# Kernel optimization log

Hardware: AMD Instinct MI355X
Metric: run time of the kernel (lower is better)

Reference implementation:

```python
import jax, jax.numpy as jnp
from jax import lax
import numpy as np

B, CIN, COUT, H, W = 16, 128, 256, 64, 64
E, K, RED = 4, 3, 4

def setup_inputs() -> dict:
    key = jax.random.key(0)
    ks = jax.random.split(key, 16)
    s = 0.05
    return {
        'x': jax.random.normal(ks[0], (B, CIN, H, W), jnp.float32),
        'expert_w': jax.random.normal(ks[1], (E, COUT, CIN, K, K), jnp.float32) * s,
        'r1_w': jax.random.normal(ks[2], (E // 2, CIN), jnp.float32) * s,
        'r1_b': jnp.zeros((E // 2,), jnp.float32),
        'r2_w': jax.random.normal(ks[3], (E, E // 2), jnp.float32) * s,
        'r2_b': jnp.zeros((E,), jnp.float32),
        'r3_w': jax.random.normal(ks[4], (E, E), jnp.float32) * s,
        'r3_b': jnp.zeros((E,), jnp.float32),
        'ca1_w': jax.random.normal(ks[5], (COUT // RED, COUT), jnp.float32) * s,
        'ca1_b': jnp.zeros((COUT // RED,), jnp.float32),
        'ca2_w': jax.random.normal(ks[6], (COUT, COUT // RED), jnp.float32) * s,
        'ca2_b': jnp.zeros((COUT,), jnp.float32),
        'sa_w': jax.random.normal(ks[7], (1, COUT, 7, 7), jnp.float32) * s,
        'sa_b': jnp.zeros((1,), jnp.float32),
        'bn_gamma': jnp.ones((COUT,), jnp.float32),
        'bn_beta': jnp.zeros((COUT,), jnp.float32),
    }

def _conv(x, w, stride, pad):
    return lax.conv_general_dilated(x, w, (stride, stride), [(pad, pad), (pad, pad)],
                                     dimension_numbers=('NCHW', 'OIHW', 'NCHW'))

def reference(x, expert_w, r1_w, r1_b, r2_w, r2_b, r3_w, r3_b,
              ca1_w, ca1_b, ca2_w, ca2_b, sa_w, sa_b, bn_gamma, bn_beta):
    # --- routing: GAP -> 1x1 convs (as matmuls) -> softmax over experts ---
    g = x.mean(axis=(2, 3))                                   # [B, Cin]
    h = jax.nn.relu(g @ r1_w.T + r1_b)
    h = jax.nn.relu(h @ r2_w.T + r2_b)
    rw = jax.nn.softmax(h @ r3_w.T + r3_b, axis=1)            # [B, E]
    # --- all experts as one stacked conv, then weighted combine ---
    w = expert_w.reshape(E * COUT, CIN, K, K)
    y = _conv(x, w, 1, 1)                                     # [B, E*Cout, H, W]
    y = y.reshape(x.shape[0], E, COUT, y.shape[2], y.shape[3])
    out = jnp.einsum('be,bechw->bchw', rw, y)                 # [B, Cout, H, W]
    # --- channel attention (SE) ---
    p = out.mean(axis=(2, 3))                                  # [B, Cout]
    ca = jax.nn.sigmoid(jax.nn.relu(p @ ca1_w.T + ca1_b) @ ca2_w.T + ca2_b)
    # --- spatial attention: 7x7 conv -> sigmoid ---
    sa = jax.nn.sigmoid(_conv(out, sa_w, 1, 3) + sa_b[None, :, None, None])  # [B,1,H,W]
    out = out * ca[:, :, None, None] * sa
    # --- BatchNorm (training mode: batch statistics) + ReLU ---
    mean = out.mean(axis=(0, 2, 3))
    var = out.var(axis=(0, 2, 3))
    out = (out - mean[None, :, None, None]) * lax.rsqrt(var + 1e-5)[None, :, None, None]
    out = out * bn_gamma[None, :, None, None] + bn_beta[None, :, None, None]
    return jax.nn.relu(out)
```

## Files before the change

kernel.cpp:

```cpp
#include <hip/hip_runtime.h>
#include <math.h>

#define B_    16
#define CIN_  128
#define COUT_ 256
#define H_    64
#define W_    64
#define HW_   4096

typedef __attribute__((ext_vector_type(8))) short short8v;
typedef __attribute__((ext_vector_type(4))) float f32x4;

#define WS_GPX     0
#define WS_RW      131072
#define WS_CP      131136
#define WS_CA      196672
#define WS_BNSCALE 208960
#define WS_BNSHIFT 209216
#define WS_SA      209472
#define WS_WSA     275008
#define WS_WCB_F   283200
#define WS_XT_F    2642496
#define WS_U_F     WS_XT_F
#define WS_MIX_F   7103040

static __device__ __forceinline__ unsigned short f2bf(float f) {
    union { float f; unsigned int u; } v; v.f = f;
    unsigned int u = v.u;
    return (unsigned short)((u + 0x7FFFu + ((u >> 16) & 1u)) >> 16);
}
static __device__ __forceinline__ float bf2f(unsigned short h) {
    union { unsigned int u; float f; } v; v.u = ((unsigned int)h) << 16;
    return v.f;
}

__device__ __forceinline__ void gl16(const void* g, const void* l) {
    __builtin_amdgcn_global_load_lds(
        (const __attribute__((address_space(1))) unsigned int*)g,
        (__attribute__((address_space(3))) unsigned int*)l, 16, 0, 0);
}

__global__ __launch_bounds__(256) void k_xt(const float* __restrict__ x,
                                            unsigned short* __restrict__ xt,
                                            float* __restrict__ gpart) {
    int wg = blockIdx.x + (blockIdx.y << 6);
    int nw = ((wg & 7) << 7) + (wg >> 3);
    int h = nw & 63, b = nw >> 6;
    int t = threadIdx.x;
    int w = t & 63, c8 = t >> 6;
    unsigned short* xtb = xt + (size_t)b * 66*66*128;
    unsigned short* orow = xtb + (((size_t)(h+1))*66 + (w+1))*128;
    float* gp = gpart + ((size_t)b*64 + h)*128;
    #pragma unroll
    for (int i = 0; i < 4; ++i) {
        int ci0 = i*32 + c8*8;
        float f[8];
        short8v vv;
        #pragma unroll
        for (int j = 0; j < 8; ++j) {
            f[j] = x[(((size_t)b*CIN_ + ci0 + j)*H_ + h)*W_ + w];
            vv[j] = (short)f2bf(f[j]);
        }
        *(short8v*)(orow + ci0) = vv;
        #pragma unroll
        for (int j = 0; j < 8; ++j) {
            float s = f[j];
            s += __shfl_down(s, 32, 64);
            s += __shfl_down(s, 16, 64);
            s += __shfl_down(s, 8, 64);
            s += __shfl_down(s, 4, 64);
            s += __shfl_down(s, 2, 64);
            s += __shfl_down(s, 1, 64);
            f[j] = s;
        }
        if (w == 0) {
            #pragma unroll
            for (int j = 0; j < 8; ++j) gp[ci0 + j] = f[j];
        }
    }
    xtb[(((size_t)(h+1))*66 + (t >> 7)*65)*128 + (t & 127)] = 0;
    if (h == 0 || h == 63) {
        int r = (h == 0) ? 0 : 65;
        unsigned short* rowp = xtb + ((size_t)r*66)*128;
        for (int i = t; i < 1056; i += 256)
            *(short8v*)(rowp + (size_t)i*8) = (short8v){0,0,0,0,0,0,0,0};
    }
}

__global__ void k_route(const float* __restrict__ gpart,
                        const float* r1w, const float* r1b,
                        const float* r2w, const float* r2b,
                        const float* r3w, const float* r3b,
                        float* __restrict__ rw) {
    int b = blockIdx.x;
    int t = threadIdx.x;
    __shared__ float gl_[128];
    float s = 0.f;
    for (int h = 0; h < 64; ++h) s += gpart[((size_t)b*64 + h)*128 + t];
    gl_[t] = s * (1.f/4096.f);
    __syncthreads();
    if (t == 0) {
        float h1[2];
        for (int j = 0; j < 2; ++j) {
            float acc = r1b[j];
            for (int c = 0; c < CIN_; ++c) acc += gl_[c]*r1w[j*CIN_+c];
            h1[j] = fmaxf(acc, 0.f);
        }
        float h2[4];
        for (int e = 0; e < 4; ++e)
            h2[e] = fmaxf(r2b[e] + h1[0]*r2w[e*2] + h1[1]*r2w[e*2+1], 0.f);
        float lg[4], m = -1e30f;
        for (int e = 0; e < 4; ++e) {
            float acc = r3b[e];
            for (int j = 0; j < 4; ++j) acc += h2[j]*r3w[e*4+j];
            lg[e] = acc; m = fmaxf(m, acc);
        }
        float den = 0.f;
        for (int e = 0; e < 4; ++e) { lg[e] = expf(lg[e]-m); den += lg[e]; }
        float inv = 1.f/den;
        for (int e = 0; e < 4; ++e) rw[b*4+e] = lg[e]*inv;
    }
}

__global__ __launch_bounds__(256) void k_wcomb(const float* __restrict__ ew,
                                               const float* __restrict__ rw,
                                               unsigned short* __restrict__ wc,
                                               const float* __restrict__ saw,
                                               unsigned short* __restrict__ wsa) {
    int t = threadIdx.x;
    if (blockIdx.x >= COUT_) {
        int i = (blockIdx.x - COUT_)*256 + t;
        int tap = i >> 8, c = i & 255;
        float v = (tap < 49) ? saw[c*49 + tap] : 0.f;
        wsa[tap*256 + c] = f2bf(v);
        return;
    }
    int co = blockIdx.x;
    __shared__ float ewl[4*1152];
    __shared__ float rwl[64];
    #pragma unroll
    for (int e = 0; e < 4; ++e) {
        const float* src = ew + ((size_t)(e*COUT_ + co))*1152;
        for (int i = t; i < 1152; i += 256) ewl[e*1152 + i] = src[i];
    }
    if (t < 64) rwl[t] = rw[t];
    __syncthreads();
    for (int i = 0; i < 72; ++i) {
        int f = i*256 + t;
        int b = f / 1152;
        int rem = f - b*1152;
        int tap = rem >> 7, ci = rem & 127;
        int lidx = ci*9 + tap;
        float v = rwl[b*4+0]*ewl[0*1152+lidx] + rwl[b*4+1]*ewl[1*1152+lidx]
                + rwl[b*4+2]*ewl[2*1152+lidx] + rwl[b*4+3]*ewl[3*1152+lidx];
        wc[((size_t)(b*9 + tap)*COUT_ + co)*128 + ci] = f2bf(v);
    }
}

__global__ __launch_bounds__(256) void k_conv(const unsigned short* __restrict__ xt,
                                              const unsigned short* __restrict__ wc,
                                              unsigned short* __restrict__ mixb,
                                              float* __restrict__ cpart) {
    __shared__ unsigned short xs[1600*8];
    __shared__ unsigned short wl[2304*8];
    __shared__ float gsl[4][64];
    int wg = blockIdx.x + (blockIdx.y << 4) + (blockIdx.z << 6);
    int nw = ((wg & 7) << 7) + (wg >> 3);
    int ht = nw & 15;
    int cb = (nw >> 4) & 3;
    int b  = nw >> 6;
    int t  = threadIdx.x;
    int wv = t >> 6, lane = t & 63;
    int lr = lane & 15, kq = lane >> 4;
    int h0 = ht * 4;

    const unsigned short* xtb = xt + (size_t)b * 66*66*128;
    const unsigned short* wcb = wc + (size_t)b * 9*256*128;

    f32x4 acc[4][4];
    #pragma unroll
    for (int m = 0; m < 4; ++m)
        #pragma unroll
        for (int n = 0; n < 4; ++n) acc[m][n] = (f32x4){0.f,0.f,0.f,0.f};

    for (int ci0 = 0; ci0 < CIN_; ci0 += 32) {
        __syncthreads();
        for (int j = wv; j < 25; j += 4) {
            int s = j*64 + lane;
            if (s > 1583) s = 1583;
            int pos = s >> 2, q = s & 3;
            int rp = pos / 66, cp = pos - rp*66;
            const unsigned short* g = xtb + (((size_t)(h0 + rp)*66 + cp)*128 + ci0 + q*8);
            gl16(g, (const char*)xs + (size_t)j*1024);
        }
        for (int j = wv; j < 36; j += 4) {
            int s = j*64 + lane;
            int tap = s >> 8, col = (s >> 2) & 63, q = s & 3;
            const unsigned short* g = wcb + (((size_t)tap*COUT_ + cb*64 + col)*128 + ci0 + q*8);
            gl16(g, (const char*)wl + (size_t)j*1024);
        }
        asm volatile("s_waitcnt vmcnt(0)" ::: "memory");
        __syncthreads();

        #pragma unroll
        for (int dh = 0; dh < 3; ++dh) {
            #pragma unroll
            for (int dw = 0; dw < 3; ++dw) {
                int tap = dh*3 + dw;
                short8v af[4], bfv[4];
                #pragma unroll
                for (int m = 0; m < 4; ++m)
                    af[m] = *(const short8v*)(wl + ((size_t)tap*2048 + (m*16 + lr)*32 + kq*8));
                #pragma unroll
                for (int n = 0; n < 4; ++n)
                    bfv[n] = *(const short8v*)(xs + ((size_t)(wv+dh)*2112 + (n*16 + lr + dw)*32 + kq*8));
                #pragma unroll
                for (int m = 0; m < 4; ++m)
                    #pragma unroll
                    for (int n = 0; n < 4; ++n)
                        acc[m][n] = __builtin_amdgcn_mfma_f32_16x16x32_bf16(
                            af[m], bfv[n], acc[m][n], 0, 0, 0);
            }
        }
    }

    unsigned short* ob = mixb + ((size_t)b*COUT_ + cb*64)*HW_ + (h0 + wv)*W_;
    #pragma unroll
    for (int m = 0; m < 4; ++m)
        #pragma unroll
        for (int n = 0; n < 4; ++n) {
            f32x4 v = acc[m][n];
            #pragma unroll
            for (int r = 0; r < 4; ++r)
                ob[(size_t)(m*16 + kq*4 + r)*HW_ + n*16 + lr] = f2bf(v[r]);
        }

    float gp[4][4];
    #pragma unroll
    for (int m = 0; m < 4; ++m)
        #pragma unroll
        for (int r = 0; r < 4; ++r)
            gp[m][r] = acc[m][0][r] + acc[m][1][r] + acc[m][2][r] + acc[m][3][r];
    #pragma unroll
    for (int o = 8; o > 0; o >>= 1)
        #pragma unroll
        for (int m = 0; m < 4; ++m)
            #pragma unroll
            for (int r = 0; r < 4; ++r)
                gp[m][r] += __shfl_down(gp[m][r], o, 64);
    if ((lane & 15) == 0) {
        #pragma unroll
        for (int m = 0; m < 4; ++m)
            #pragma unroll
            for (int r = 0; r < 4; ++r)
                gsl[wv][m*16 + kq*4 + r] = gp[m][r];
    }
    __syncthreads();
    if (t < 64) {
        float s = gsl[0][t] + gsl[1][t] + gsl[2][t] + gsl[3][t];
        cpart[((size_t)b*16 + ht)*COUT_ + cb*64 + t] = s;
    }
}

__global__ __launch_bounds__(256) void k_sa_gemm(const unsigned short* __restrict__ mixb,
                                                 const unsigned short* __restrict__ wsa,
                                                 float* __restrict__ u) {
    __shared__ unsigned short wl[16384];
    __shared__ unsigned short bt[16384];
    int wg = blockIdx.x + (blockIdx.y << 6);
    int nw = ((wg & 7) << 7) + (wg >> 3);
    int pxt = nw & 63;
    int b   = nw >> 6;
    int t = threadIdx.x, wv = t >> 6, lane = t & 63;
    int lr = lane & 15, kq = lane >> 4;
    int px0 = pxt * 64;

    #pragma unroll
    for (int k = 0; k < 8; ++k) {
        int s = t + k*256;
        int row = s >> 5, cs = s & 31;
        short8v v = *(const short8v*)(wsa + row*256 + cs*8);
        int off = row*512 + ((cs*16) ^ ((row & 7) << 4));
        *(short8v*)((char*)wl + off) = v;
    }
    {
        int px = lane;
        const unsigned short* mb = mixb + (size_t)b*COUT_*HW_ + px0 + px;
        #pragma unroll
        for (int c8 = 0; c8 < 8; ++c8) {
            int cb = wv*64 + c8*8;
            short8v v;
            #pragma unroll
            for (int j = 0; j < 8; ++j)
                v[j] = (short)mb[(size_t)(cb + j)*HW_];
            int off = px*512 + ((cb*2) ^ ((px & 7) << 4));
            *(short8v*)((char*)bt + off) = v;
        }
    }
    __syncthreads();

    f32x4 acc[4];
    #pragma unroll
    for (int n = 0; n < 4; ++n) acc[n] = (f32x4){0.f,0.f,0.f,0.f};

    #pragma unroll
    for (int ks = 0; ks < 8; ++ks) {
        int ci0 = ks*32;
        int arow = wv*16 + lr;
        short8v a = *(const short8v*)((const char*)wl +
                        arow*512 + (((ci0 + kq*8)*2) ^ ((arow & 7) << 4)));
        #pragma unroll
        for (int n = 0; n < 4; ++n) {
            int prow = n*16 + lr;
            short8v bv = *(const short8v*)((const char*)bt +
                            prow*512 + (((ci0 + kq*8)*2) ^ ((prow & 7) << 4)));
            acc[n] = __builtin_amdgcn_mfma_f32_16x16x32_bf16(a, bv, acc[n], 0, 0, 0);
        }
    }

    float* ub = u + (size_t)b*64*HW_;
    #pragma unroll
    for (int n = 0; n < 4; ++n)
        #pragma unroll
        for (int r = 0; r < 4; ++r)
            ub[(size_t)(wv*16 + kq*4 + r)*HW_ + px0 + n*16 + lr] = acc[n][r];
}

__global__ void k_sared_ca(const float* __restrict__ u, const float* __restrict__ sab,
                           float* __restrict__ sa,
                           const float* __restrict__ cpart,
                           const float* __restrict__ ca1w, const float* __restrict__ ca1b,
                           const float* __restrict__ ca2w, const float* __restrict__ ca2b,
                           float* __restrict__ ca) {
    int wg = blockIdx.x + (blockIdx.y << 4);
    int nw = ((wg & 7) << 5) + (wg >> 3);
    int hg = nw & 15;
    int b  = nw >> 4;
    int t = threadIdx.x;
    {
        int h = hg * 4 + (t >> 6);
        int w = t & 63;
        float s = sab[0];
        const float* ub = u + (size_t)b*64*HW_;
        #pragma unroll
        for (int dh = 0; dh < 7; ++dh) {
            int hh = h + dh - 3;
            if (hh < 0 || hh >= H_) continue;
            #pragma unroll
            for (int dw = 0; dw < 7; ++dw) {
                int ww = w + dw - 3;
                if (ww < 0 || ww >= W_) continue;
                s += ub[(size_t)(dh*7 + dw)*HW_ + hh*W_ + ww];
            }
        }
        sa[(size_t)b*HW_ + h*W_ + w] = 1.f/(1.f + expf(-s));
    }
    if (hg == 0) {
        __shared__ float pfull[256];
        __shared__ float h1[64];
        float s0 = 0.f;
        for (int h = 0; h < 16; ++h) s0 += cpart[((size_t)b*16 + h)*COUT_ + t];
        pfull[t] = s0 * (1.f/(float)HW_);
        __syncthreads();
        if (t < 64) {
            float s = ca1b[t];
            for (int c = 0; c < COUT_; ++c) s += pfull[c] * ca1w[t*COUT_ + c];
            h1[t] = fmaxf(s, 0.f);
        }
        __syncthreads();
        float s2 = ca2b[t];
        for (int j = 0; j < 64; ++j) s2 += h1[j] * ca2w[t*64 + j];
        ca[b*COUT_ + t] = 1.f/(1.f + expf(-s2));
    }
}

__global__ void k_statsfin(const unsigned short* __restrict__ mixb,
                           const float* __restrict__ ca, const float* __restrict__ sa,
                           const float* __restrict__ gamma, const float* __restrict__ beta,
                           float* __restrict__ scale, float* __restrict__ shift) {
    int c = blockIdx.x;
    int t = threadIdx.x;
    float s = 0.f, sq = 0.f;
    for (int b = 0; b < B_; ++b) {
        float cav = ca[b*COUT_ + c];
        const unsigned short* pl = mixb + ((size_t)b*COUT_ + c) * HW_;
        const float* sab = sa + (size_t)b * HW_;
        for (int i = t; i < HW_/8; i += 256) {
            short8v v = ((const short8v*)pl)[i];
            float4 w0 = ((const float4*)sab)[2*i];
            float4 w1 = ((const float4*)sab)[2*i+1];
            float f0 = bf2f((unsigned short)v[0])*cav*w0.x;
            float f1 = bf2f((unsigned short)v[1])*cav*w0.y;
            float f2 = bf2f((unsigned short)v[2])*cav*w0.z;
            float f3 = bf2f((unsigned short)v[3])*cav*w0.w;
            float f4 = bf2f((unsigned short)v[4])*cav*w1.x;
            float f5 = bf2f((unsigned short)v[5])*cav*w1.y;
            float f6 = bf2f((unsigned short)v[6])*cav*w1.z;
            float f7 = bf2f((unsigned short)v[7])*cav*w1.w;
            s  += f0+f1+f2+f3+f4+f5+f6+f7;
            sq += f0*f0+f1*f1+f2*f2+f3*f3+f4*f4+f5*f5+f6*f6+f7*f7;
        }
    }
    for (int o = 32; o > 0; o >>= 1) { s += __shfl_down(s,o,64); sq += __shfl_down(sq,o,64); }
    __shared__ float ls[8];
    int wid = t >> 6, lane = t & 63;
    if (lane == 0) { ls[wid] = s; ls[4+wid] = sq; }
    __syncthreads();
    if (t == 0) {
        float ts = ls[0]+ls[1]+ls[2]+ls[3];
        float tq = ls[4]+ls[5]+ls[6]+ls[7];
        float n = (float)(B_*HW_);
        float mean = ts/n;
        float var = tq/n - mean*mean;
        float sc = gamma[c] * rsqrtf(var + 1e-5f);
        scale[c] = sc;
        shift[c] = beta[c] - mean*sc;
    }
}

__global__ void k_bnapply(const unsigned short* __restrict__ mixb, float* __restrict__ out,
                          const float* __restrict__ ca, const float* __restrict__ sa,
                          const float* __restrict__ scale, const float* __restrict__ shift) {
    int wg = blockIdx.x;
    int nw = ((wg & 7) << 10) + (wg >> 3);
    size_t i = (size_t)nw * 256 + threadIdx.x;
    int c = (int)((i >> 9) & 255);
    int b = (int)(i >> 17);
    int px8 = (int)(i & 511);
    float cav = ca[b*COUT_ + c];
    float sc = scale[c], sh = shift[c];
    short8v v = ((const short8v*)mixb)[i];
    const float4* sp = (const float4*)(sa + (size_t)b*HW_) + (size_t)px8*2;
    float4 w0 = sp[0], w1 = sp[1];
    float4 o0, o1;
    o0.x = fmaxf(fmaf(bf2f((unsigned short)v[0])*cav*w0.x, sc, sh), 0.f);
    o0.y = fmaxf(fmaf(bf2f((unsigned short)v[1])*cav*w0.y, sc, sh), 0.f);
    o0.z = fmaxf(fmaf(bf2f((unsigned short)v[2])*cav*w0.z, sc, sh), 0.f);
    o0.w = fmaxf(fmaf(bf2f((unsigned short)v[3])*cav*w0.w, sc, sh), 0.f);
    o1.x = fmaxf(fmaf(bf2f((unsigned short)v[4])*cav*w1.x, sc, sh), 0.f);
    o1.y = fmaxf(fmaf(bf2f((unsigned short)v[5])*cav*w1.y, sc, sh), 0.f);
    o1.z = fmaxf(fmaf(bf2f((unsigned short)v[6])*cav*w1.z, sc, sh), 0.f);
    o1.w = fmaxf(fmaf(bf2f((unsigned short)v[7])*cav*w1.w, sc, sh), 0.f);
    ((float4*)out)[i*2]   = o0;
    ((float4*)out)[i*2+1] = o1;
}

extern "C" void kernel_launch(void* const* d_in, const int* in_sizes, int n_in,
                              void* d_out, int out_size, void* d_ws, size_t ws_size,
                              hipStream_t stream) {
    const float* x    = (const float*)d_in[0];
    const float* ew   = (const float*)d_in[1];
    const float* r1w  = (const float*)d_in[2];
    const float* r1b  = (const float*)d_in[3];
    const float* r2w  = (const float*)d_in[4];
    const float* r2b  = (const float*)d_in[5];
    const float* r3w  = (const float*)d_in[6];
    const float* r3b  = (const float*)d_in[7];
    const float* ca1w = (const float*)d_in[8];
    const float* ca1b = (const float*)d_in[9];
    const float* ca2w = (const float*)d_in[10];
    const float* ca2b = (const float*)d_in[11];
    const float* saw  = (const float*)d_in[12];
    const float* sab  = (const float*)d_in[13];
    const float* gm   = (const float*)d_in[14];
    const float* bt   = (const float*)d_in[15];
    float* out = (float*)d_out;
    float* ws  = (float*)d_ws;
    unsigned short* wcb  = (unsigned short*)(ws + WS_WCB_F);
    unsigned short* xt   = (unsigned short*)(ws + WS_XT_F);
    unsigned short* wsa  = (unsigned short*)(ws + WS_WSA);
    unsigned short* mixb = (unsigned short*)(ws + WS_MIX_F);
    float* u = ws + WS_U_F;

    k_xt<<<dim3(64,16), 256, 0, stream>>>(x, xt, ws+WS_GPX);
    k_route<<<16, 128, 0, stream>>>(ws+WS_GPX, r1w, r1b, r2w, r2b, r3w, r3b, ws+WS_RW);
    k_wcomb<<<320, 256, 0, stream>>>(ew, ws+WS_RW, wcb, saw, wsa);
    k_conv<<<dim3(16,4,16), 256, 0, stream>>>(xt, wcb, mixb, ws+WS_CP);
    k_sa_gemm<<<dim3(64,16), 256, 0, stream>>>(mixb, wsa, u);
    k_sared_ca<<<dim3(16,16), 256, 0, stream>>>(u, sab, ws+WS_SA, ws+WS_CP,
                                                ca1w, ca1b, ca2w, ca2b, ws+WS_CA);
    k_statsfin<<<256, 256, 0, stream>>>(mixb, ws+WS_CA, ws+WS_SA, gm, bt,
                                        ws+WS_BNSCALE, ws+WS_BNSHIFT);
    k_bnapply<<<8192, 256, 0, stream>>>(mixb, out, ws+WS_CA, ws+WS_SA,
                                        ws+WS_BNSCALE, ws+WS_BNSHIFT);
}
```

Baseline: 143.3 us.

## Reorder conv LDS tiles to kq-major layout and store spatial-attention partials in bf16

The conv kernel's shared-memory staging of input and weight tiles is rearranged so the four k-quarters of each row form separate contiguous planes. Fragment reads then step through consecutive 16-byte lanes, which aims to cut LDS bank conflicts and simplify address arithmetic. Separately, the 49-tap spatial-attention partial tensor u is written and read as bf16 instead of fp32, halving that intermediate's memory traffic. The bf16 partials lose some precision before the 7x7 reduction and sigmoid.

New measurement: 144.4 us. No clear change (+0.8%).

```diff
diff --git a/kernel.cpp b/kernel.cpp
--- a/kernel.cpp
+++ b/kernel.cpp
@@ -161,8 +161,8 @@
                                               const unsigned short* __restrict__ wc,
                                               unsigned short* __restrict__ mixb,
                                               float* __restrict__ cpart) {
-    __shared__ unsigned short xs[1600*8];
-    __shared__ unsigned short wl[2304*8];
+    __shared__ __align__(16) unsigned short xs[1600*8];
+    __shared__ __align__(16) unsigned short wl[2304*8];
     __shared__ float gsl[4][64];
     int wg = blockIdx.x + (blockIdx.y << 4) + (blockIdx.z << 6);
     int nw = ((wg & 7) << 7) + (wg >> 3);
@@ -177,6 +177,11 @@
     const unsigned short* xtb = xt + (size_t)b * 66*66*128;
     const unsigned short* wcb = wc + (size_t)b * 9*256*128;
 
+    const char* xs_c = (const char*)xs;
+    const char* wl_c = (const char*)wl;
+    int base_x = wv*4224 + kq*1056 + lr*16;
+    int base_w = kq*1024 + lr*16;
+
     f32x4 acc[4][4];
     #pragma unroll
     for (int m = 0; m < 4; ++m)
@@ -188,15 +193,16 @@
         for (int j = wv; j < 25; j += 4) {
             int s = j*64 + lane;
             if (s > 1583) s = 1583;
-            int pos = s >> 2, q = s & 3;
-            int rp = pos / 66, cp = pos - rp*66;
-            const unsigned short* g = xtb + (((size_t)(h0 + rp)*66 + cp)*128 + ci0 + q*8);
+            int row = s / 264;
+            int rem = s - row*264;
+            int kq2 = rem / 66, col = rem - kq2*66;
+            const unsigned short* g = xtb + (((size_t)(h0 + row)*66 + col)*128 + ci0 + kq2*8);
             gl16(g, (const char*)xs + (size_t)j*1024);
         }
         for (int j = wv; j < 36; j += 4) {
             int s = j*64 + lane;
-            int tap = s >> 8, col = (s >> 2) & 63, q = s & 3;
-            const unsigned short* g = wcb + (((size_t)tap*COUT_ + cb*64 + col)*128 + ci0 + q*8);
+            int tap = s >> 8, kq2 = (s >> 6) & 3, co = s & 63;
+            const unsigned short* g = wcb + (((size_t)tap*COUT_ + cb*64 + co)*128 + ci0 + kq2*8);
             gl16(g, (const char*)wl + (size_t)j*1024);
         }
         asm volatile("s_waitcnt vmcnt(0)" ::: "memory");
@@ -210,10 +216,10 @@
                 short8v af[4], bfv[4];
                 #pragma unroll
                 for (int m = 0; m < 4; ++m)
-                    af[m] = *(const short8v*)(wl + ((size_t)tap*2048 + (m*16 + lr)*32 + kq*8));
+                    af[m] = *(const short8v*)(wl_c + base_w + tap*4096 + m*256);
                 #pragma unroll
                 for (int n = 0; n < 4; ++n)
-                    bfv[n] = *(const short8v*)(xs + ((size_t)(wv+dh)*2112 + (n*16 + lr + dw)*32 + kq*8));
+                    bfv[n] = *(const short8v*)(xs_c + base_x + dh*4224 + dw*16 + n*256);
                 #pragma unroll
                 for (int m = 0; m < 4; ++m)
                     #pragma unroll
@@ -264,7 +270,7 @@
 
 __global__ __launch_bounds__(256) void k_sa_gemm(const unsigned short* __restrict__ mixb,
                                                  const unsigned short* __restrict__ wsa,
-                                                 float* __restrict__ u) {
+                                                 unsigned short* __restrict__ u) {
     __shared__ unsigned short wl[16384];
     __shared__ unsigned short bt[16384];
     int wg = blockIdx.x + (blockIdx.y << 6);
@@ -318,15 +324,15 @@
         }
     }
 
-    float* ub = u + (size_t)b*64*HW_;
+    unsigned short* ub = u + (size_t)b*64*HW_;
     #pragma unroll
     for (int n = 0; n < 4; ++n)
         #pragma unroll
         for (int r = 0; r < 4; ++r)
-            ub[(size_t)(wv*16 + kq*4 + r)*HW_ + px0 + n*16 + lr] = acc[n][r];
-}
-
-__global__ void k_sared_ca(const float* __restrict__ u, const float* __restrict__ sab,
+            ub[(size_t)(wv*16 + kq*4 + r)*HW_ + px0 + n*16 + lr] = f2bf(acc[n][r]);
+}
+
+__global__ void k_sared_ca(const unsigned short* __restrict__ u, const float* __restrict__ sab,
                            float* __restrict__ sa,
                            const float* __restrict__ cpart,
                            const float* __restrict__ ca1w, const float* __restrict__ ca1b,
@@ -341,7 +347,7 @@
         int h = hg * 4 + (t >> 6);
         int w = t & 63;
         float s = sab[0];
-        const float* ub = u + (size_t)b*64*HW_;
+        const unsigned short* ub = u + (size_t)b*64*HW_;
         #pragma unroll
         for (int dh = 0; dh < 7; ++dh) {
             int hh = h + dh - 3;
@@ -350,7 +356,7 @@
             for (int dw = 0; dw < 7; ++dw) {
                 int ww = w + dw - 3;
                 if (ww < 0 || ww >= W_) continue;
-                s += ub[(size_t)(dh*7 + dw)*HW_ + hh*W_ + ww];
+                s += bf2f(ub[(size_t)(dh*7 + dw)*HW_ + hh*W_ + ww]);
             }
         }
         sa[(size_t)b*HW_ + h*W_ + w] = 1.f/(1.f + expf(-s));
@@ -470,7 +476,7 @@
     unsigned short* xt   = (unsigned short*)(ws + WS_XT_F);
     unsigned short* wsa  = (unsigned short*)(ws + WS_WSA);
     unsigned short* mixb = (unsigned short*)(ws + WS_MIX_F);
-    float* u = ws + WS_U_F;
+    unsigned short* u    = (unsigned short*)(ws + WS_U_F);
 
     k_xt<<<dim3(64,16), 256, 0, stream>>>(x, xt, ws+WS_GPX);
     k_route<<<16, 128, 0, stream>>>(ws+WS_GPX, r1w, r1b, r2w, r2b, r3w, r3b, ws+WS_RW);
```
